# Kernel optimization log

Hardware: AMD Instinct MI355X
Metric: run time of the kernel (lower is better)

## Reference

```python
import jax, jax.numpy as jnp
import numpy as np

B, N, DIM = 2, 2048, 2048
H, DH = 16, 128            # heads, dim_head; dim_inner = H*DH = 2048
SOFTCAP = 50.0
SCALE = DH ** -0.5


def setup_inputs() -> dict:
    key = jax.random.key(0)
    k1, k2, k3, k4 = jax.random.split(key, 4)
    s = 1.0 / np.sqrt(DIM)
    x = jax.random.normal(k1, (B, N, DIM), dtype=jnp.float32)
    w_qkv = jax.random.normal(k2, (DIM, 3 * H * DH), dtype=jnp.float32) * s
    w_gates = jax.random.normal(k3, (DIM, H), dtype=jnp.float32) * s
    w_out = jax.random.normal(k4, (H * DH, DIM), dtype=jnp.float32) * s
    return {"x": x, "w_qkv": w_qkv, "w_gates": w_gates, "w_out": w_out}


def reference(x, w_qkv, w_gates, w_out):
    b, n, _ = x.shape
    # to_qkv: Linear then 'b n (qkv h d) -> qkv b h n d'
    qkv = (x @ w_qkv).reshape(b, n, 3, H, DH).transpose(2, 0, 3, 1, 4)
    q, k, v = qkv[0], qkv[1], qkv[2]            # each [b, h, n, d]
    q = q * SCALE
    sim = jnp.einsum('bhid,bhjd->bhij', q, k)   # [b, h, n, n]
    sim = jnp.tanh(sim / SOFTCAP) * SOFTCAP     # softclamp
    mask_value = -jnp.finfo(sim.dtype).max
    causal_mask = jnp.triu(jnp.ones((n, n), dtype=bool), 1)
    sim = jnp.where(causal_mask, mask_value, sim)
    attn = jax.nn.softmax(sim, axis=-1)         # dropout = 0.0 (eval)
    out = jnp.einsum('bhij,bhjd->bhid', attn, v)
    # gating: 'b n h -> b h n 1' then sigmoid
    gates = jax.nn.sigmoid(x @ w_gates)         # [b, n, h]
    out = out * gates.transpose(0, 2, 1)[..., None]
    # to_out: 'b h n d -> b n (h d)' then Linear
    out = out.transpose(0, 2, 1, 3).reshape(b, n, H * DH) @ w_out
    return out
```

## Files before the change

### kernel.cpp

```cpp
#include <hip/hip_runtime.h>
#include <hip/hip_bf16.h>
#include <math.h>


typedef __attribute__((ext_vector_type(8))) __bf16 bf16x8;
typedef __attribute__((ext_vector_type(4))) __bf16 bf16x4;
typedef __attribute__((ext_vector_type(4))) float f32x4;

#define MFMA_BF16(a, b, c) __builtin_amdgcn_mfma_f32_16x16x32_bf16((a), (b), (c), 0, 0, 0)

#define NB 2
#define NSEQ 2048
#define NDIM 2048
#define NH 16
#define NDH 128
#define SCALE_Q 0.08838834764831845f

#define AS1 __attribute__((address_space(1)))
#define AS3 __attribute__((address_space(3)))
static __device__ __forceinline__ void gload_lds16(const void* g, void* l) {
  __builtin_amdgcn_global_load_lds((AS1 const void*)g, (AS3 void*)l, 16, 0, 0);
}

static __device__ __forceinline__ unsigned pack2_bf16(float a, float b) {
  unsigned short ua = __builtin_bit_cast(unsigned short, (__bf16)a);
  unsigned short ub = __builtin_bit_cast(unsigned short, (__bf16)b);
  return (unsigned)ua | ((unsigned)ub << 16);
}

__global__ __launch_bounds__(256) void cvt_gates_kernel(const float* __restrict__ x,
                                                        const float* __restrict__ wg,
                                                        __bf16* __restrict__ x_bf,
                                                        float* __restrict__ gates) {
  __shared__ float red[64];
  int row = blockIdx.x;
  int tid = threadIdx.x;
  const float* xr = x + (size_t)row * NDIM;
  int k0 = tid * 8;
  float4 v0 = *reinterpret_cast<const float4*>(xr + k0);
  float4 v1 = *reinterpret_cast<const float4*>(xr + k0 + 4);
  float vv[8] = {v0.x, v0.y, v0.z, v0.w, v1.x, v1.y, v1.z, v1.w};
  union { bf16x8 v; } o;
#pragma unroll
  for (int j = 0; j < 8; ++j) o.v[j] = (__bf16)vv[j];
  *reinterpret_cast<bf16x8*>(x_bf + (size_t)row * NDIM + k0) = o.v;

  float acc[16];
#pragma unroll
  for (int h = 0; h < 16; ++h) acc[h] = 0.f;
#pragma unroll
  for (int j = 0; j < 8; ++j) {
    const float* wr = wg + (size_t)(k0 + j) * NH;
#pragma unroll
    for (int h = 0; h < 16; ++h) acc[h] += vv[j] * wr[h];
  }
  int w = tid >> 6, lane = tid & 63;
#pragma unroll
  for (int h = 0; h < 16; ++h) {
    float v = acc[h];
#pragma unroll
    for (int off = 32; off; off >>= 1) v += __shfl_down(v, off);
    if (lane == 0) red[w * 16 + h] = v;
  }
  __syncthreads();
  if (tid < 16) {
    float s = red[tid] + red[16 + tid] + red[32 + tid] + red[48 + tid];
    int b = row >> 11, n = row & 2047;
    gates[((size_t)(b * NH + tid)) * NSEQ + n] = 1.f / (1.f + expf(-s));
  }
}

__global__ __launch_bounds__(256) void transpose_cvt_kernel(const float* __restrict__ in,
                                                            __bf16* __restrict__ out,
                                                            int K, int C) {
  __shared__ float tile[32][33];
  int c0 = blockIdx.x * 32, k0 = blockIdx.y * 32;
  int t = threadIdx.x;
  int lc = t & 31, lr = t >> 5;
#pragma unroll
  for (int rr = 0; rr < 4; ++rr)
    tile[lr + rr * 8][lc] = in[(size_t)(k0 + lr + rr * 8) * C + c0 + lc];
  __syncthreads();
#pragma unroll
  for (int rr = 0; rr < 4; ++rr)
    out[(size_t)(c0 + lr + rr * 8) * K + k0 + lc] = (__bf16)tile[lc][lr + rr * 8];
}

struct SmemQ4 {
  __bf16 T[4][640][32];
};

static __device__ __forceinline__ const bf16x8* fragq(const __bf16* base, int row, int g) {
  return (const bf16x8*)(base + row * 32 + (g ^ ((row >> 1) & 3)) * 8);
}

__global__ __launch_bounds__(512, 2) void gemm_qkv256b(const __bf16* __restrict__ A,
                                                       const __bf16* __restrict__ Bt,
                                                       __bf16* __restrict__ qb,
                                                       __bf16* __restrict__ kb,
                                                       __bf16* __restrict__ vtb) {
  __shared__ __align__(1024) SmemQ4 S;
  int sblk = blockIdx.x;
  int x = sblk & 7, i = sblk >> 3;
  int m0 = (i >> 1) * 256;
  int n0 = (2 * x + (i & 1)) * 384;
  const __bf16* Ab = A + (size_t)m0 * 2048;
  const __bf16* Bb = Bt + (size_t)n0 * 2048;

  int tid = threadIdx.x;
  int w = tid >> 6, lane = tid & 63;
  int ln15 = lane & 15, g = lane >> 4;
  int wr = w >> 2, wc = w & 3;
  int lr4 = lane >> 2, l3 = lane & 3;

  auto stage = [&](int kt, int rb) {
#pragma unroll
    for (int j = 0; j < 5; ++j) {
      int k = w + 8 * j;
      int row = k * 16 + lr4;
      int sg = l3 ^ ((row >> 1) & 3);
      const __bf16* src = (k < 16)
          ? Ab + (size_t)row * 2048 + kt * 32 + sg * 8
          : Bb + (size_t)(row - 256) * 2048 + kt * 32 + sg * 8;
      gload_lds16(src, &S.T[rb][k * 16][0]);
    }
  };

  f32x4 acc[8][6];
#pragma unroll
  for (int a = 0; a < 8; ++a)
#pragma unroll
    for (int nf = 0; nf < 6; ++nf) acc[a][nf] = (f32x4){0.f, 0.f, 0.f, 0.f};

  stage(0, 0);
  stage(1, 1);
  stage(2, 2);
  for (int t = 0; t < 64; ++t) {
    int rb = t & 3;
    asm volatile("s_waitcnt vmcnt(10)" ::: "memory");
    __builtin_amdgcn_s_barrier();
    asm volatile("" ::: "memory");
    int ts = (t < 61) ? t + 3 : 63;
    stage(ts, (t + 3) & 3);
    const __bf16* Sb = &S.T[rb][0][0];
    bf16x8 bfr[6];
#pragma unroll
    for (int nf = 0; nf < 6; ++nf) {
      int row = 256 + wc * 96 + nf * 16 + ln15;
      bfr[nf] = *fragq(Sb, row, g);
    }
#pragma unroll
    for (int mh = 0; mh < 2; ++mh) {
      bf16x8 af[4];
#pragma unroll
      for (int a = 0; a < 4; ++a) {
        int row = wr * 128 + (mh * 4 + a) * 16 + ln15;
        af[a] = *fragq(Sb, row, g);
      }
      __builtin_amdgcn_s_setprio(1);
#pragma unroll
      for (int a = 0; a < 4; ++a)
#pragma unroll
        for (int nf = 0; nf < 6; ++nf)
          acc[mh * 4 + a][nf] = MFMA_BF16(af[a], bfr[nf], acc[mh * 4 + a][nf]);
      __builtin_amdgcn_s_setprio(0);
    }
  }
  asm volatile("s_waitcnt vmcnt(0)" ::: "memory");

#pragma unroll
  for (int nf = 0; nf < 6; ++nf) {
    int ng = n0 + wc * 96 + nf * 16 + ln15;
    int qkv = ng >> 11;
    int h = (ng >> 7) & 15;
    int d = ng & 127;
#pragma unroll
    for (int mf = 0; mf < 8; ++mf)
#pragma unroll
      for (int rr = 0; rr < 4; ++rr) {
        int m = m0 + wr * 128 + mf * 16 + g * 4 + rr;
        int b = m >> 11, n = m & 2047;
        int bh = b * NH + h;
        float v = acc[mf][nf][rr];
        if (qkv == 0)
          qb[((size_t)bh * NSEQ + n) * NDH + d] = (__bf16)(v * SCALE_Q);
        else if (qkv == 1)
          kb[((size_t)bh * NSEQ + n) * NDH + d] = (__bf16)v;
        else
          vtb[((size_t)bh * NDH + d) * NSEQ + n] = (__bf16)v;
      }
  }
}

struct SmemO {
  __bf16 T[6][384][32];
};

__global__ __launch_bounds__(512, 2) void gemm_out256r(const __bf16* __restrict__ A,
                                                       const __bf16* __restrict__ Bt,
                                                       float* __restrict__ out) {
  __shared__ __align__(1024) SmemO S;
  int sblk = blockIdx.x;
  int x = sblk & 7, i = sblk >> 3;
  int m0 = (i >> 1) * 256;
  int n0 = (2 * x + (i & 1)) * 128;
  const __bf16* Ab = A + (size_t)m0 * 2048;
  const __bf16* Bb = Bt + (size_t)n0 * 2048;

  int tid = threadIdx.x;
  int w = tid >> 6, lane = tid & 63;
  int ln15 = lane & 15, g = lane >> 4;
  int wr = w >> 2, wc = w & 3;
  int lr4 = lane >> 2, l3 = lane & 3;

  auto stage = [&](int kt, int rb) {
#pragma unroll
    for (int j = 0; j < 3; ++j) {
      int k = w + 8 * j;
      int row = k * 16 + lr4;
      int sg = l3 ^ ((row >> 1) & 3);
      const __bf16* src = (k < 16)
          ? Ab + (size_t)row * 2048 + kt * 32 + sg * 8
          : Bb + (size_t)(row - 256) * 2048 + kt * 32 + sg * 8;
      gload_lds16(src, &S.T[rb][k * 16][0]);
    }
  };

  f32x4 acc[8][2];
#pragma unroll
  for (int a = 0; a < 8; ++a)
#pragma unroll
    for (int nf = 0; nf < 2; ++nf) acc[a][nf] = (f32x4){0.f, 0.f, 0.f, 0.f};

  stage(0, 0);
  stage(1, 1);
  stage(2, 2);
  stage(3, 3);
  stage(4, 4);
  for (int t = 0; t < 64; ++t) {
    int rb = t % 6;
    asm volatile("s_waitcnt vmcnt(12)" ::: "memory");
    __builtin_amdgcn_s_barrier();
    asm volatile("" ::: "memory");
    int ts = (t < 59) ? t + 5 : 63;
    stage(ts, (t + 5) % 6);
    const __bf16* Sb = &S.T[rb][0][0];
    bf16x8 bfr[2];
#pragma unroll
    for (int nf = 0; nf < 2; ++nf) {
      int row = 256 + wc * 32 + nf * 16 + ln15;
      bfr[nf] = *fragq(Sb, row, g);
    }
#pragma unroll
    for (int mh = 0; mh < 2; ++mh) {
      bf16x8 af[4];
#pragma unroll
      for (int a = 0; a < 4; ++a) {
        int row = wr * 128 + (mh * 4 + a) * 16 + ln15;
        af[a] = *fragq(Sb, row, g);
      }
      __builtin_amdgcn_s_setprio(1);
#pragma unroll
      for (int a = 0; a < 4; ++a)
#pragma unroll
        for (int nf = 0; nf < 2; ++nf)
          acc[mh * 4 + a][nf] = MFMA_BF16(af[a], bfr[nf], acc[mh * 4 + a][nf]);
      __builtin_amdgcn_s_setprio(0);
    }
  }
  asm volatile("s_waitcnt vmcnt(0)" ::: "memory");

#pragma unroll
  for (int mf = 0; mf < 8; ++mf)
#pragma unroll
    for (int nf = 0; nf < 2; ++nf)
#pragma unroll
      for (int rr = 0; rr < 4; ++rr) {
        int m = m0 + wr * 128 + mf * 16 + g * 4 + rr;
        int c = n0 + wc * 32 + nf * 16 + ln15;
        out[(size_t)m * NDIM + c] = acc[mf][nf][rr];
      }
}

static __device__ __forceinline__ void softcap_p(const f32x4* accS, float (*p)[4],
                                                 float& l_r, int j0, int q0s,
                                                 bool diag, int ln15, int g) {
#pragma unroll
  for (int jt = 0; jt < 4; ++jt)
#pragma unroll
    for (int r = 0; r < 4; ++r) {
      float e2 = __builtin_amdgcn_exp2f(accS[jt][r] * 0.057707801635558536f);
      float rc = __builtin_amdgcn_rcpf(e2 + 1.f);
      float pv = __builtin_amdgcn_exp2f(fmaf(rc, -144.26950408889634f, 54.82241155378061f));
      if (diag && (j0 + jt * 16 + g * 4 + r > q0s + ln15)) pv = 0.f;
      p[jt][r] = pv;
      l_r += pv;
    }
}

static __device__ __forceinline__ bf16x8 build_pa(const float (*p)[4], int c,
                                                  int lane_lo, int lane_hi, int g) {
  unsigned P0w0 = pack2_bf16(p[2 * c][0], p[2 * c][1]);
  unsigned P0w1 = pack2_bf16(p[2 * c][2], p[2 * c][3]);
  unsigned P1w0 = pack2_bf16(p[2 * c + 1][0], p[2 * c + 1][1]);
  unsigned P1w1 = pack2_bf16(p[2 * c + 1][2], p[2 * c + 1][3]);
  unsigned a0 = (unsigned)__shfl((int)P0w0, lane_lo);
  unsigned a1 = (unsigned)__shfl((int)P0w1, lane_lo);
  unsigned b0 = (unsigned)__shfl((int)P1w0, lane_lo);
  unsigned b1 = (unsigned)__shfl((int)P1w1, lane_lo);
  unsigned c0 = (unsigned)__shfl((int)P0w0, lane_hi);
  unsigned c1 = (unsigned)__shfl((int)P0w1, lane_hi);
  unsigned e0 = (unsigned)__shfl((int)P1w0, lane_hi);
  unsigned e1 = (unsigned)__shfl((int)P1w1, lane_hi);
  union { unsigned u[4]; bf16x8 v; } pu;
  pu.u[0] = (g < 2) ? a0 : b0;
  pu.u[1] = (g < 2) ? a1 : b1;
  pu.u[2] = (g < 2) ? c0 : e0;
  pu.u[3] = (g < 2) ? c1 : e1;
  return pu.v;
}

static __device__ __forceinline__ void attn_tile2(const __bf16* __restrict__ Kl,
                                                  const __bf16* __restrict__ Vl,
                                                  const bf16x8* qfh, const bf16x8* qfl,
                                                  f32x4* acc_h, f32x4* acc_l,
                                                  float& l_h, float& l_l,
                                                  int j0, int q0h, int q0l,
                                                  bool diag_h, bool diag_l, bool do_lo,
                                                  int ln15, int g) {
  f32x4 sh[4], sl[4];
#pragma unroll
  for (int jt = 0; jt < 4; ++jt) {
    sh[jt] = (f32x4){0.f, 0.f, 0.f, 0.f};
    sl[jt] = (f32x4){0.f, 0.f, 0.f, 0.f};
  }
  __builtin_amdgcn_s_setprio(1);
#pragma unroll
  for (int jt = 0; jt < 4; ++jt)
#pragma unroll
    for (int kc = 0; kc < 4; ++kc) {
      int row = jt * 16 + ln15;
      int bc = (kc * 64 + g * 16) ^ ((row & 7) << 4);
      bf16x8 kf = *reinterpret_cast<const bf16x8*>(Kl + row * 128 + (bc >> 1));
      sh[jt] = MFMA_BF16(kf, qfh[kc], sh[jt]);
      if (do_lo) sl[jt] = MFMA_BF16(kf, qfl[kc], sl[jt]);
    }
  __builtin_amdgcn_s_setprio(0);
  float ph[4][4], pl[4][4];
  softcap_p(sh, ph, l_h, j0, q0h, diag_h, ln15, g);
  if (do_lo) softcap_p(sl, pl, l_l, j0, q0l, diag_l, ln15, g);
  int lane_lo = ln15 + 32 * (g & 1);
  int lane_hi = lane_lo + 16;
#pragma unroll
  for (int c = 0; c < 2; ++c) {
    bf16x8 pah = build_pa(ph, c, lane_lo, lane_hi, g);
    bf16x8 pal = build_pa(pl, c, lane_lo, lane_hi, g);
    __builtin_amdgcn_s_setprio(1);
#pragma unroll
    for (int d0 = 0; d0 < 8; ++d0) {
      int d = d0 * 16 + ln15;
      int bc = (c * 64 + g * 16) ^ ((d & 7) << 4);
      bf16x8 vf = *reinterpret_cast<const bf16x8*>(Vl + d * 64 + (bc >> 1));
      acc_h[d0] = MFMA_BF16(pah, vf, acc_h[d0]);
      if (do_lo) acc_l[d0] = MFMA_BF16(pal, vf, acc_l[d0]);
    }
    __builtin_amdgcn_s_setprio(0);
  }
}

__global__ __launch_bounds__(256, 2) void attn_kernel(const __bf16* __restrict__ qb,
                                                      const __bf16* __restrict__ kb,
                                                      const __bf16* __restrict__ vtb,
                                                      const float* __restrict__ gates,
                                                      __bf16* __restrict__ og) {
  __shared__ __align__(1024) __bf16 Kl[2][64 * 128];
  __shared__ __align__(1024) __bf16 Vl[2][128 * 64];
  int tid = threadIdx.x;
  int w = tid >> 6, lane = tid & 63;
  int ln15 = lane & 15, g = lane >> 4;
  int bx = blockIdx.x;
  int lo = bx & 15, bh = bx >> 4;
  int hi = 31 - lo;
  const __bf16* qh = qb + (size_t)bh * NSEQ * NDH;
  const __bf16* kh = kb + (size_t)bh * NSEQ * NDH;
  const __bf16* vh = vtb + (size_t)bh * NDH * NSEQ;

  int q0h = hi * 64 + w * 16;
  int q0l = lo * 64 + w * 16;
  bf16x8 qfh[4], qfl[4];
#pragma unroll
  for (int kc = 0; kc < 4; ++kc) {
    qfh[kc] = *reinterpret_cast<const bf16x8*>(qh + (size_t)(q0h + ln15) * NDH + kc * 32 + g * 8);
    qfl[kc] = *reinterpret_cast<const bf16x8*>(qh + (size_t)(q0l + ln15) * NDH + kc * 32 + g * 8);
  }

  f32x4 acc_h[8], acc_l[8];
#pragma unroll
  for (int d0 = 0; d0 < 8; ++d0) {
    acc_h[d0] = (f32x4){0.f, 0.f, 0.f, 0.f};
    acc_l[d0] = (f32x4){0.f, 0.f, 0.f, 0.f};
  }
  float l_h = 0.f, l_l = 0.f;

  auto stage = [&](int t, int buf) {
    int j0 = t * 64;
#pragma unroll
    for (int i = 0; i < 4; ++i) {
      int gi = (i * 4 + w) * 64 + lane;
      int kr = gi >> 4, kcs = gi & 15;
      int kc_ = kcs ^ (kr & 7);
      gload_lds16(kh + (size_t)(j0 + kr) * NDH + kc_ * 8, &Kl[buf][(i * 4 + w) * 512]);
      int vr = gi >> 3, vcs = gi & 7;
      int vc_ = vcs ^ (vr & 7);
      gload_lds16(vh + (size_t)vr * NSEQ + j0 + vc_ * 8, &Vl[buf][(i * 4 + w) * 512]);
    }
  };

  stage(0, 0);
  for (int t = 0; t <= hi; ++t) {
    int cb = t & 1;
    if (t < hi) {
      stage(t + 1, cb ^ 1);
      asm volatile("s_waitcnt vmcnt(8)" ::: "memory");
    } else {
      asm volatile("s_waitcnt vmcnt(0)" ::: "memory");
    }
    __builtin_amdgcn_s_barrier();
    attn_tile2(&Kl[cb][0], &Vl[cb][0], qfh, qfl, acc_h, acc_l, l_h, l_l,
               t * 64, q0h, q0l, t == hi, t == lo, t <= lo, ln15, g);
    __builtin_amdgcn_s_barrier();
  }

  l_h += __shfl_xor(l_h, 16); l_h += __shfl_xor(l_h, 32);
  l_l += __shfl_xor(l_l, 16); l_l += __shfl_xor(l_l, 32);

  int b = bh >> 4, h = bh & 15;
#pragma unroll
  for (int set = 0; set < 2; ++set) {
    int q0s = set ? q0l : q0h;
    f32x4* acc = set ? acc_l : acc_h;
    float lr = set ? l_l : l_h;
    float gv[4];
#pragma unroll
    for (int r = 0; r < 4; ++r) {
      float lv = __shfl(lr, g * 4 + r);
      int row = q0s + g * 4 + r;
      gv[r] = gates[(size_t)bh * NSEQ + row] / lv;
    }
#pragma unroll
    for (int d0 = 0; d0 < 8; ++d0)
#pragma unroll
      for (int r = 0; r < 4; ++r) {
        int row = q0s + g * 4 + r;
        og[((size_t)(b * NSEQ + row)) * NDIM + h * NDH + d0 * 16 + ln15] =
            (__bf16)(acc[d0][r] * gv[r]);
      }
  }
}

extern "C" void kernel_launch(void* const* d_in, const int* in_sizes, int n_in,
                              void* d_out, int out_size, void* d_ws, size_t ws_size,
                              hipStream_t stream) {
  const float* x = (const float*)d_in[0];
  const float* w_qkv = (const float*)d_in[1];
  const float* w_gates = (const float*)d_in[2];
  const float* w_out = (const float*)d_in[3];
  float* out = (float*)d_out;
  char* ws = (char*)d_ws;

  __bf16* x_bf   = (__bf16*)(ws + 0);
  __bf16* wqkv_t = (__bf16*)(ws + 16777216);
  __bf16* wout_t = (__bf16*)(ws + 41943040);
  __bf16* q_buf  = (__bf16*)(ws + 50331648);
  __bf16* k_buf  = (__bf16*)(ws + 67108864);
  __bf16* vt_buf = (__bf16*)(ws + 83886080);
  float*  gates  = (float*)(ws + 100663296);
  __bf16* attn_g = (__bf16*)(ws + 100925440);

  cvt_gates_kernel<<<4096, 256, 0, stream>>>(x, w_gates, x_bf, gates);
  transpose_cvt_kernel<<<dim3(192, 64), 256, 0, stream>>>(w_qkv, wqkv_t, 2048, 6144);
  transpose_cvt_kernel<<<dim3(64, 64), 256, 0, stream>>>(w_out, wout_t, 2048, 2048);
  gemm_qkv256b<<<256, 512, 0, stream>>>(x_bf, wqkv_t, q_buf, k_buf, vt_buf);
  attn_kernel<<<512, 256, 0, stream>>>(q_buf, k_buf, vt_buf, gates, attn_g);
  gemm_out256r<<<256, 512, 0, stream>>>(attn_g, wout_t, out);
}
```

Before: 341.0 us.

## Rewrite QKV GEMM with 256x256 tiles, K=64 double buffering and phased staging

Replaces the 256x384-tile, K=32, 4-stage QKV GEMM with a 256x256-tile kernel that uses K=64 slices, separate double-buffered A/B LDS arrays and an XOR swizzle. Each k-step is split into four phases that interleave LDS fragment reads, partial global-to-LDS staging and MFMA bursts, with barriers between them. The grid grows from 256 to 384 blocks for better CU coverage. The cost is more barriers per iteration and a shallower prefetch depth, which may expose memory latency.

```diff
diff --git a/kernel.cpp b/kernel.cpp
--- a/kernel.cpp
+++ b/kernel.cpp
@@ -86,24 +86,17 @@
     out[(size_t)(c0 + lr + rr * 8) * K + k0 + lc] = (__bf16)tile[lc][lr + rr * 8];
 }
 
-struct SmemQ4 {
-  __bf16 T[4][640][32];
-};
-
-static __device__ __forceinline__ const bf16x8* fragq(const __bf16* base, int row, int g) {
-  return (const bf16x8*)(base + row * 32 + (g ^ ((row >> 1) & 3)) * 8);
-}
-
-__global__ __launch_bounds__(512, 2) void gemm_qkv256b(const __bf16* __restrict__ A,
-                                                       const __bf16* __restrict__ Bt,
-                                                       __bf16* __restrict__ qb,
-                                                       __bf16* __restrict__ kb,
-                                                       __bf16* __restrict__ vtb) {
-  __shared__ __align__(1024) SmemQ4 S;
+__global__ __launch_bounds__(512, 2) void gemm_qkv8p(const __bf16* __restrict__ A,
+                                                     const __bf16* __restrict__ Bt,
+                                                     __bf16* __restrict__ qb,
+                                                     __bf16* __restrict__ kb,
+                                                     __bf16* __restrict__ vtb) {
+  __shared__ __align__(1024) __bf16 SA[2][256][64];
+  __shared__ __align__(1024) __bf16 SB[2][256][64];
   int sblk = blockIdx.x;
   int x = sblk & 7, i = sblk >> 3;
-  int m0 = (i >> 1) * 256;
-  int n0 = (2 * x + (i & 1)) * 384;
+  int n0 = (3 * x + (i % 3)) * 256;
+  int m0 = (i / 3) * 256;
   const __bf16* Ab = A + (size_t)m0 * 2048;
   const __bf16* Bb = Bt + (size_t)n0 * 2048;
 
@@ -111,66 +104,85 @@
   int w = tid >> 6, lane = tid & 63;
   int ln15 = lane & 15, g = lane >> 4;
   int wr = w >> 2, wc = w & 3;
-  int lr4 = lane >> 2, l3 = lane & 3;
-
-  auto stage = [&](int kt, int rb) {
-#pragma unroll
-    for (int j = 0; j < 5; ++j) {
-      int k = w + 8 * j;
-      int row = k * 16 + lr4;
-      int sg = l3 ^ ((row >> 1) & 3);
-      const __bf16* src = (k < 16)
-          ? Ab + (size_t)row * 2048 + kt * 32 + sg * 8
-          : Bb + (size_t)(row - 256) * 2048 + kt * 32 + sg * 8;
-      gload_lds16(src, &S.T[rb][k * 16][0]);
-    }
+  int l8 = lane >> 3, l7 = lane & 7;
+  int sg = l7 ^ l8;
+
+  auto stage_aq = [&](int kt, int q, int bf) {
+    int rb = (w >> 2) * 128 + q * 32 + (w & 3) * 8;
+    int row = rb + l8;
+    gload_lds16(Ab + (size_t)row * 2048 + kt * 64 + sg * 8, &SA[bf][rb][0]);
   };
-
-  f32x4 acc[8][6];
+  auto stage_bh = [&](int kt, int h, int bf) {
+#pragma unroll
+    for (int j = 0; j < 2; ++j) {
+      int rb = h * 128 + j * 64 + w * 8;
+      int row = rb + l8;
+      gload_lds16(Bb + (size_t)row * 2048 + kt * 64 + sg * 8, &SB[bf][rb][0]);
+    }
+  };
+
+  f32x4 acc[8][4];
 #pragma unroll
   for (int a = 0; a < 8; ++a)
 #pragma unroll
-    for (int nf = 0; nf < 6; ++nf) acc[a][nf] = (f32x4){0.f, 0.f, 0.f, 0.f};
-
-  stage(0, 0);
-  stage(1, 1);
-  stage(2, 2);
-  for (int t = 0; t < 64; ++t) {
-    int rb = t & 3;
-    asm volatile("s_waitcnt vmcnt(10)" ::: "memory");
-    __builtin_amdgcn_s_barrier();
-    asm volatile("" ::: "memory");
-    int ts = (t < 61) ? t + 3 : 63;
-    stage(ts, (t + 3) & 3);
-    const __bf16* Sb = &S.T[rb][0][0];
-    bf16x8 bfr[6];
-#pragma unroll
-    for (int nf = 0; nf < 6; ++nf) {
-      int row = 256 + wc * 96 + nf * 16 + ln15;
-      bfr[nf] = *fragq(Sb, row, g);
-    }
-#pragma unroll
-    for (int mh = 0; mh < 2; ++mh) {
-      bf16x8 af[4];
-#pragma unroll
-      for (int a = 0; a < 4; ++a) {
-        int row = wr * 128 + (mh * 4 + a) * 16 + ln15;
-        af[a] = *fragq(Sb, row, g);
-      }
+    for (int nf = 0; nf < 4; ++nf) acc[a][nf] = (f32x4){0.f, 0.f, 0.f, 0.f};
+
+  stage_aq(0, 0, 0); stage_aq(0, 1, 0); stage_aq(0, 2, 0); stage_aq(0, 3, 0);
+  stage_bh(0, 0, 0); stage_bh(0, 1, 0);
+  stage_aq(1, 0, 1); stage_aq(1, 1, 1); stage_aq(1, 2, 1);
+  stage_bh(1, 0, 1); stage_bh(1, 1, 1);
+  asm volatile("s_waitcnt vmcnt(7)" ::: "memory");
+  __builtin_amdgcn_s_barrier();
+
+  bf16x8 bfr[4][2], af2[2][2];
+  for (int t = 0; t < 32; ++t) {
+    int bf = t & 1;
+    const __bf16* sa = &SA[bf][0][0];
+    const __bf16* sb = &SB[bf][0][0];
+    int kt1 = (t + 1 < 32) ? t + 1 : 31;
+    int kt2 = (t + 2 < 32) ? t + 2 : 31;
+#pragma unroll
+    for (int p = 0; p < 4; ++p) {
+      if (p == 0) {
+#pragma unroll
+        for (int nf = 0; nf < 4; ++nf) {
+          int r = wc * 64 + nf * 16 + ln15;
+          bfr[nf][0] = *(const bf16x8*)(sb + r * 64 + ((g) ^ (r & 7)) * 8);
+          bfr[nf][1] = *(const bf16x8*)(sb + r * 64 + ((4 | g) ^ (r & 7)) * 8);
+        }
+      }
+#pragma unroll
+      for (int f = 0; f < 2; ++f) {
+        int r = wr * 128 + (2 * p + f) * 16 + ln15;
+        af2[f][0] = *(const bf16x8*)(sa + r * 64 + ((g) ^ (r & 7)) * 8);
+        af2[f][1] = *(const bf16x8*)(sa + r * 64 + ((4 | g) ^ (r & 7)) * 8);
+      }
+      if (p == 0) stage_aq(kt1, 3, bf ^ 1);
+      if (p == 1) { stage_aq(kt2, 0, bf); stage_bh(kt2, 0, bf); }
+      if (p == 2) { stage_aq(kt2, 1, bf); stage_bh(kt2, 1, bf); }
+      if (p == 3) stage_aq(kt2, 2, bf);
+      __builtin_amdgcn_s_barrier();
+      asm volatile("s_waitcnt lgkmcnt(0)" ::: "memory");
+      __builtin_amdgcn_sched_barrier(0);
       __builtin_amdgcn_s_setprio(1);
 #pragma unroll
-      for (int a = 0; a < 4; ++a)
-#pragma unroll
-        for (int nf = 0; nf < 6; ++nf)
-          acc[mh * 4 + a][nf] = MFMA_BF16(af[a], bfr[nf], acc[mh * 4 + a][nf]);
+      for (int f = 0; f < 2; ++f)
+#pragma unroll
+        for (int nf = 0; nf < 4; ++nf) {
+          acc[2 * p + f][nf] = MFMA_BF16(af2[f][0], bfr[nf][0], acc[2 * p + f][nf]);
+          acc[2 * p + f][nf] = MFMA_BF16(af2[f][1], bfr[nf][1], acc[2 * p + f][nf]);
+        }
       __builtin_amdgcn_s_setprio(0);
+      if (p == 3)
+        asm volatile("s_waitcnt vmcnt(7)" ::: "memory");
+      __builtin_amdgcn_s_barrier();
     }
   }
   asm volatile("s_waitcnt vmcnt(0)" ::: "memory");
 
 #pragma unroll
-  for (int nf = 0; nf < 6; ++nf) {
-    int ng = n0 + wc * 96 + nf * 16 + ln15;
+  for (int nf = 0; nf < 4; ++nf) {
+    int ng = n0 + wc * 64 + nf * 16 + ln15;
     int qkv = ng >> 11;
     int h = (ng >> 7) & 15;
     int d = ng & 127;
@@ -196,6 +208,10 @@
   __bf16 T[6][384][32];
 };
 
+static __device__ __forceinline__ const bf16x8* fragq(const __bf16* base, int row, int g) {
+  return (const bf16x8*)(base + row * 32 + (g ^ ((row >> 1) & 3)) * 8);
+}
+
 __global__ __launch_bounds__(512, 2) void gemm_out256r(const __bf16* __restrict__ A,
                                                        const __bf16* __restrict__ Bt,
                                                        float* __restrict__ out) {
@@ -232,11 +248,7 @@
 #pragma unroll
     for (int nf = 0; nf < 2; ++nf) acc[a][nf] = (f32x4){0.f, 0.f, 0.f, 0.f};
 
-  stage(0, 0);
-  stage(1, 1);
-  stage(2, 2);
-  stage(3, 3);
-  stage(4, 4);
+  stage(0, 0); stage(1, 1); stage(2, 2); stage(3, 3); stage(4, 4);
   for (int t = 0; t < 64; ++t) {
     int rb = t % 6;
     asm volatile("s_waitcnt vmcnt(12)" ::: "memory");
@@ -480,7 +492,7 @@
   cvt_gates_kernel<<<4096, 256, 0, stream>>>(x, w_gates, x_bf, gates);
   transpose_cvt_kernel<<<dim3(192, 64), 256, 0, stream>>>(w_qkv, wqkv_t, 2048, 6144);
   transpose_cvt_kernel<<<dim3(64, 64), 256, 0, stream>>>(w_out, wout_t, 2048, 2048);
-  gemm_qkv256b<<<256, 512, 0, stream>>>(x_bf, wqkv_t, q_buf, k_buf, vt_buf);
+  gemm_qkv8p<<<384, 512, 0, stream>>>(x_bf, wqkv_t, q_buf, k_buf, vt_buf);
   attn_kernel<<<512, 256, 0, stream>>>(q_buf, k_buf, vt_buf, gates, attn_g);
   gemm_out256r<<<256, 512, 0, stream>>>(attn_g, wout_t, out);
 }
```

After: 391.1 us. 1.15x slower.

## Restructure QKV GEMM pipeline into triple-buffered interleaved load/compute phases

Applied to the files above, without the earlier changes.

The QKV projection GEMM goes from a 4-deep LDS ring with one barrier per k-step to a 3-deep ring. Each k-step is split into two half-phases, and the global-to-LDS loads for the next stage are interleaved between the fragment reads and the MFMA bursts, separated by extra barriers. The aim is to cut LDS footprint, which could help occupancy, and to spread memory issue evenly across the compute. The cost is more barriers per iteration and less prefetch depth, which may expose more memory latency.

```diff
diff --git a/kernel.cpp b/kernel.cpp
--- a/kernel.cpp
+++ b/kernel.cpp
@@ -86,20 +86,20 @@
     out[(size_t)(c0 + lr + rr * 8) * K + k0 + lc] = (__bf16)tile[lc][lr + rr * 8];
 }
 
-struct SmemQ4 {
-  __bf16 T[4][640][32];
+struct SmemQ {
+  __bf16 T[3][640][32];
 };
 
 static __device__ __forceinline__ const bf16x8* fragq(const __bf16* base, int row, int g) {
   return (const bf16x8*)(base + row * 32 + (g ^ ((row >> 1) & 3)) * 8);
 }
 
-__global__ __launch_bounds__(512, 2) void gemm_qkv256b(const __bf16* __restrict__ A,
-                                                       const __bf16* __restrict__ Bt,
-                                                       __bf16* __restrict__ qb,
-                                                       __bf16* __restrict__ kb,
-                                                       __bf16* __restrict__ vtb) {
-  __shared__ __align__(1024) SmemQ4 S;
+__global__ __launch_bounds__(512, 2) void gemm_qkv2p(const __bf16* __restrict__ A,
+                                                     const __bf16* __restrict__ Bt,
+                                                     __bf16* __restrict__ qb,
+                                                     __bf16* __restrict__ kb,
+                                                     __bf16* __restrict__ vtb) {
+  __shared__ __align__(1024) SmemQ S;
   int sblk = blockIdx.x;
   int x = sblk & 7, i = sblk >> 3;
   int m0 = (i >> 1) * 256;
@@ -113,18 +113,19 @@
   int wr = w >> 2, wc = w & 3;
   int lr4 = lane >> 2, l3 = lane & 3;
 
-  auto stage = [&](int kt, int rb) {
-#pragma unroll
-    for (int j = 0; j < 5; ++j) {
-      int k = w + 8 * j;
-      int row = k * 16 + lr4;
-      int sg = l3 ^ ((row >> 1) & 3);
-      const __bf16* src = (k < 16)
-          ? Ab + (size_t)row * 2048 + kt * 32 + sg * 8
-          : Bb + (size_t)(row - 256) * 2048 + kt * 32 + sg * 8;
-      gload_lds16(src, &S.T[rb][k * 16][0]);
-    }
+  auto stage1 = [&](int kt, int rb, int j) {
+    int k = w + 8 * j;
+    int row = k * 16 + lr4;
+    int sg = l3 ^ ((row >> 1) & 3);
+    const __bf16* src = (k < 16)
+        ? Ab + (size_t)row * 2048 + kt * 32 + sg * 8
+        : Bb + (size_t)(row - 256) * 2048 + kt * 32 + sg * 8;
+    gload_lds16(src, &S.T[rb][k * 16][0]);
   };
+  auto stage_all = [&](int kt, int rb) {
+#pragma unroll
+    for (int j = 0; j < 5; ++j) stage1(kt, rb, j);
+  };
 
   f32x4 acc[8][6];
 #pragma unroll
@@ -132,39 +133,52 @@
 #pragma unroll
     for (int nf = 0; nf < 6; ++nf) acc[a][nf] = (f32x4){0.f, 0.f, 0.f, 0.f};
 
-  stage(0, 0);
-  stage(1, 1);
-  stage(2, 2);
+  stage_all(0, 0);
+  stage_all(1, 1);
+  asm volatile("s_waitcnt vmcnt(5)" ::: "memory");
+  __builtin_amdgcn_s_barrier();
   for (int t = 0; t < 64; ++t) {
-    int rb = t & 3;
-    asm volatile("s_waitcnt vmcnt(10)" ::: "memory");
-    __builtin_amdgcn_s_barrier();
-    asm volatile("" ::: "memory");
-    int ts = (t < 61) ? t + 3 : 63;
-    stage(ts, (t + 3) & 3);
+    int rb = t % 3;
+    int ts = (t < 62) ? t + 2 : 63;
+    int sb = (t + 2) % 3;
     const __bf16* Sb = &S.T[rb][0][0];
-    bf16x8 bfr[6];
+    bf16x8 bfr[6], af[4];
 #pragma unroll
     for (int nf = 0; nf < 6; ++nf) {
       int row = 256 + wc * 96 + nf * 16 + ln15;
       bfr[nf] = *fragq(Sb, row, g);
     }
 #pragma unroll
-    for (int mh = 0; mh < 2; ++mh) {
-      bf16x8 af[4];
-#pragma unroll
-      for (int a = 0; a < 4; ++a) {
-        int row = wr * 128 + (mh * 4 + a) * 16 + ln15;
-        af[a] = *fragq(Sb, row, g);
-      }
-      __builtin_amdgcn_s_setprio(1);
-#pragma unroll
-      for (int a = 0; a < 4; ++a)
-#pragma unroll
-        for (int nf = 0; nf < 6; ++nf)
-          acc[mh * 4 + a][nf] = MFMA_BF16(af[a], bfr[nf], acc[mh * 4 + a][nf]);
-      __builtin_amdgcn_s_setprio(0);
-    }
+    for (int a = 0; a < 4; ++a) {
+      int row = wr * 128 + a * 16 + ln15;
+      af[a] = *fragq(Sb, row, g);
+    }
+    stage1(ts, sb, 0); stage1(ts, sb, 1); stage1(ts, sb, 2);
+    __builtin_amdgcn_s_barrier();
+    __builtin_amdgcn_s_setprio(1);
+#pragma unroll
+    for (int a = 0; a < 4; ++a)
+#pragma unroll
+      for (int nf = 0; nf < 6; ++nf)
+        acc[a][nf] = MFMA_BF16(af[a], bfr[nf], acc[a][nf]);
+    __builtin_amdgcn_s_setprio(0);
+    __builtin_amdgcn_s_barrier();
+#pragma unroll
+    for (int a = 0; a < 4; ++a) {
+      int row = wr * 128 + (a + 4) * 16 + ln15;
+      af[a] = *fragq(Sb, row, g);
+    }
+    stage1(ts, sb, 3); stage1(ts, sb, 4);
+    __builtin_amdgcn_s_barrier();
+    __builtin_amdgcn_s_setprio(1);
+#pragma unroll
+    for (int a = 0; a < 4; ++a)
+#pragma unroll
+      for (int nf = 0; nf < 6; ++nf)
+        acc[a + 4][nf] = MFMA_BF16(af[a], bfr[nf], acc[a + 4][nf]);
+    __builtin_amdgcn_s_setprio(0);
+    asm volatile("s_waitcnt vmcnt(5)" ::: "memory");
+    __builtin_amdgcn_s_barrier();
   }
   asm volatile("s_waitcnt vmcnt(0)" ::: "memory");
 
@@ -232,11 +246,7 @@
 #pragma unroll
     for (int nf = 0; nf < 2; ++nf) acc[a][nf] = (f32x4){0.f, 0.f, 0.f, 0.f};
 
-  stage(0, 0);
-  stage(1, 1);
-  stage(2, 2);
-  stage(3, 3);
-  stage(4, 4);
+  stage(0, 0); stage(1, 1); stage(2, 2); stage(3, 3); stage(4, 4);
   for (int t = 0; t < 64; ++t) {
     int rb = t % 6;
     asm volatile("s_waitcnt vmcnt(12)" ::: "memory");
@@ -480,7 +490,7 @@
   cvt_gates_kernel<<<4096, 256, 0, stream>>>(x, w_gates, x_bf, gates);
   transpose_cvt_kernel<<<dim3(192, 64), 256, 0, stream>>>(w_qkv, wqkv_t, 2048, 6144);
   transpose_cvt_kernel<<<dim3(64, 64), 256, 0, stream>>>(w_out, wout_t, 2048, 2048);
-  gemm_qkv256b<<<256, 512, 0, stream>>>(x_bf, wqkv_t, q_buf, k_buf, vt_buf);
+  gemm_qkv2p<<<256, 512, 0, stream>>>(x_bf, wqkv_t, q_buf, k_buf, vt_buf);
   attn_kernel<<<512, 256, 0, stream>>>(q_buf, k_buf, vt_buf, gates, attn_g);
   gemm_out256r<<<256, 512, 0, stream>>>(attn_g, wout_t, out);
 }
```

Measured after the change: 340.9 us. Within noise of the previous version (-0.0%).
